# Kernel optimization log

Hardware: AMD Instinct MI355X
Metric: run time of the kernel (lower is better)

## Reference

```python
import jax, jax.numpy as jnp
import numpy as np


def _tet_geometry(vertices, indices, tet_density):
    """Gather 4 corners per tet, compute area (|det|/6), min edge length, alpha."""
    v = vertices[indices]                      # [T,4,3]
    v0, v1, v2, v3 = v[:, 0], v[:, 1], v[:, 2], v[:, 3]
    # --- tet area: |det([v1-v0, v2-v0, v3-v0])| / 6 ---
    e1, e2, e3 = v1 - v0, v2 - v0, v3 - v0     # [T,3] each
    det = (e1[:, 0] * (e2[:, 1] * e3[:, 2] - e2[:, 2] * e3[:, 1])
           - e1[:, 1] * (e2[:, 0] * e3[:, 2] - e2[:, 2] * e3[:, 0])
           + e1[:, 2] * (e2[:, 0] * e3[:, 1] - e2[:, 1] * e3[:, 0]))
    tet_area = jnp.abs(det) / 6.0              # [T]
    # --- edge lengths of all 6 edges, take min (mode='min') ---
    edge_sq = jnp.stack([
        jnp.sum((v0 - v1) ** 2, axis=1),
        jnp.sum((v0 - v2) ** 2, axis=1),
        jnp.sum((v0 - v3) ** 2, axis=1),
        jnp.sum((v1 - v2) ** 2, axis=1),
        jnp.sum((v1 - v3) ** 2, axis=1),
        jnp.sum((v2 - v3) ** 2, axis=1),
    ], axis=0)                                 # [6,T]
    el = jnp.sqrt(jnp.min(edge_sq, axis=0))    # [T]
    tet_alpha = 1.0 - jnp.exp(-tet_density * el)
    return tet_area, tet_alpha


def _vert_density(tet_density, indices, num_verts):
    # torch scatter_reduce_ 'amax' with zero-initialized dest and include_self=True
    # == segment_max over all 4 corner slots, clamped below at 0.
    flat_idx = indices.reshape(-1)                         # [4T]
    src = jnp.repeat(tet_density, 4)                       # [4T], matches row-major flatten
    vmax = jax.ops.segment_max(src, flat_idx, num_segments=num_verts)
    return jnp.maximum(vmax, jnp.zeros((), vmax.dtype))    # untouched verts -> 0


def setup_inputs() -> dict:
    key = jax.random.key(0)
    k1, k2, k3 = jax.random.split(key, 3)
    V, T = 1_000_000, 4_000_000
    vertices = jax.random.normal(k1, (V, 3), dtype=jnp.float32)
    indices = jax.random.randint(k2, (T, 4), 0, V, dtype=jnp.int32)
    tet_density = jax.random.uniform(k3, (T,), dtype=jnp.float32)
    return {"vertices": vertices, "indices": indices, "tet_density": tet_density}


def reference(vertices, indices, tet_density):
    tet_area, tet_alpha = _tet_geometry(vertices, indices, tet_density)
    vert_density = _vert_density(tet_density, indices, vertices.shape[0])
    return tet_area, tet_alpha, vert_density
```

## Files before the change

kernel.cpp:

```cpp
#include <hip/hip_runtime.h>

typedef int nt_int4 __attribute__((ext_vector_type(4)));

#define NB     256
#define VSHIFT 12
#define BMASK  ((1 << VSHIFT) - 1)
#define BCAP   65536
#define RT     4
#define NR     4


__global__ __launch_bounds__(256) void setup_kernel(uint4* __restrict__ vd4, int n4,
                                                    unsigned* __restrict__ gcnt,
                                                    const float* __restrict__ verts,
                                                    float4* __restrict__ verts4, int V) {
    int i = blockIdx.x * blockDim.x + threadIdx.x;
    if (i < n4) vd4[i] = make_uint4(0u, 0u, 0u, 0u);
    if (gcnt && i < NB) gcnt[i] = 0u;
    if (verts4 && i < V) {
        const float* p = verts + (size_t)i * 3;
        verts4[i] = make_float4(p[0], p[1], p[2], 0.f);
    }
}

__global__ __launch_bounds__(256) void fused_geom_bin_kernel(
    const float4* __restrict__ verts4,
    const int4*  __restrict__ idx4,
    const float* __restrict__ dens,
    float* __restrict__ out_area,
    float* __restrict__ out_alpha,
    unsigned*    __restrict__ pairs,
    unsigned*    __restrict__ gcnt,
    unsigned*    __restrict__ vd,
    int T)
{
    __shared__ unsigned s_cnt[NB];
    __shared__ unsigned s_run[NB];
    __shared__ unsigned s_roff[NB];
    __shared__ unsigned s_wc[NB];
    __shared__ unsigned s_wsum[4];
    __shared__ uint2    stage[256 * RT * 4];

    int tid  = threadIdx.x;
    int lane = tid & 63;
    int wid  = tid >> 6;
    int base = blockIdx.x * (256 * RT * NR);

    s_cnt[tid] = 0u;
    __syncthreads();
    for (int k = 0; k < RT * NR; ++k) {
        int i = base + k * 256 + tid;
        if (i < T) {
            int4 q = idx4[i];
            atomicAdd(&s_cnt[(unsigned)q.x >> VSHIFT], 1u);
            atomicAdd(&s_cnt[(unsigned)q.y >> VSHIFT], 1u);
            atomicAdd(&s_cnt[(unsigned)q.z >> VSHIFT], 1u);
            atomicAdd(&s_cnt[(unsigned)q.w >> VSHIFT], 1u);
        }
    }
    __syncthreads();

    s_run[tid] = atomicAdd(&gcnt[tid], s_cnt[tid]);
    __syncthreads();

    for (int r = 0; r < NR; ++r) {
        int4  q[RT];
        float dd[RT];
        bool  vl[RT];
#pragma unroll
        for (int k = 0; k < RT; ++k) {
            int i = base + (r * RT + k) * 256 + tid;
            vl[k] = (i < T);
            if (vl[k]) { q[k] = idx4[i]; dd[k] = dens[i]; }
        }

#pragma unroll
        for (int k = 0; k < RT; ++k) if (vl[k]) {
            int i = base + (r * RT + k) * 256 + tid;
            float4 v0 = verts4[q[k].x];
            float4 v1 = verts4[q[k].y];
            float4 v2 = verts4[q[k].z];
            float4 v3 = verts4[q[k].w];

            float e1x = v1.x - v0.x, e1y = v1.y - v0.y, e1z = v1.z - v0.z;
            float e2x = v2.x - v0.x, e2y = v2.y - v0.y, e2z = v2.z - v0.z;
            float e3x = v3.x - v0.x, e3y = v3.y - v0.y, e3z = v3.z - v0.z;

            float det = e1x * (e2y * e3z - e2z * e3y)
                      - e1y * (e2x * e3z - e2z * e3x)
                      + e1z * (e2x * e3y - e2y * e3x);
            __builtin_nontemporal_store(fabsf(det) * (1.0f / 6.0f), &out_area[i]);

            float q01 = e1x * e1x + e1y * e1y + e1z * e1z;
            float q02 = e2x * e2x + e2y * e2y + e2z * e2z;
            float q03 = e3x * e3x + e3y * e3y + e3z * e3z;
            float ax, ay, az;
            ax = v1.x - v2.x; ay = v1.y - v2.y; az = v1.z - v2.z;
            float q12 = ax * ax + ay * ay + az * az;
            ax = v1.x - v3.x; ay = v1.y - v3.y; az = v1.z - v3.z;
            float q13 = ax * ax + ay * ay + az * az;
            ax = v2.x - v3.x; ay = v2.y - v3.y; az = v2.z - v3.z;
            float q23 = ax * ax + ay * ay + az * az;

            float mn = fminf(fminf(fminf(q01, q02), fminf(q03, q12)), fminf(q13, q23));
            float el = sqrtf(mn);
            __builtin_nontemporal_store(1.0f - expf(-dd[k] * el), &out_alpha[i]);
        }

        s_cnt[tid] = 0u;
        __syncthreads();
#pragma unroll
        for (int k = 0; k < RT; ++k) if (vl[k]) {
            atomicAdd(&s_cnt[(unsigned)q[k].x >> VSHIFT], 1u);
            atomicAdd(&s_cnt[(unsigned)q[k].y >> VSHIFT], 1u);
            atomicAdd(&s_cnt[(unsigned)q[k].z >> VSHIFT], 1u);
            atomicAdd(&s_cnt[(unsigned)q[k].w >> VSHIFT], 1u);
        }
        __syncthreads();

        unsigned x = s_cnt[tid];
        unsigned incl = x;
#pragma unroll
        for (int s = 1; s < 64; s <<= 1) {
            unsigned t = __shfl_up(incl, s);
            if (lane >= s) incl += t;
        }
        if (lane == 63) s_wsum[wid] = incl;
        __syncthreads();
        unsigned pre = 0;
#pragma unroll
        for (int w = 0; w < 4; ++w) pre += (w < wid) ? s_wsum[w] : 0u;
        unsigned npairs = s_wsum[0] + s_wsum[1] + s_wsum[2] + s_wsum[3];
        s_roff[tid] = pre + incl - x;
        s_wc[tid]   = 0u;
        __syncthreads();

#pragma unroll
        for (int k = 0; k < RT; ++k) if (vl[k]) {
            unsigned db = __float_as_uint(dd[k]);
            unsigned vv[4] = { (unsigned)q[k].x, (unsigned)q[k].y,
                               (unsigned)q[k].z, (unsigned)q[k].w };
#pragma unroll
            for (int j = 0; j < 4; ++j) {
                unsigned b    = vv[j] >> VSHIFT;
                unsigned slot = s_roff[b] + atomicAdd(&s_wc[b], 1u);
                stage[slot] = make_uint2(vv[j], db);
            }
        }
        __syncthreads();

        for (unsigned l = tid; l < npairs; l += 256) {
            uint2 e = stage[l];
            unsigned b  = e.x >> VSHIFT;
            unsigned rr = s_run[b] + (l - s_roff[b]);
            if (rr < BCAP) {
                unsigned w = ((e.x & BMASK) << 20) | (e.y >> 12);
                __builtin_nontemporal_store(w, pairs + (size_t)b * BCAP + rr);
            } else {
                atomicMax(vd + e.x, e.y);
            }
        }
        __syncthreads();

        s_run[tid] += s_cnt[tid];
    }
}

__global__ __launch_bounds__(1024) void bucket_max_kernel(
    const unsigned* __restrict__ pairs,
    const unsigned* __restrict__ gcnt,
    unsigned*       __restrict__ vd,
    int V)
{
    __shared__ unsigned tbl[1 << VSHIFT];
    int b   = blockIdx.x;
    int tid = threadIdx.x;

    for (int j = tid; j < (1 << VSHIFT); j += 1024) tbl[j] = 0u;
    __syncthreads();

    unsigned cnt = gcnt[b];
    if (cnt > BCAP) cnt = BCAP;
    const unsigned* p = pairs + (size_t)b * BCAP;
    const uint4* p4 = (const uint4*)p;
    unsigned n4c = cnt >> 2;
    for (unsigned i = tid; i < n4c; i += 1024) {
        uint4 e = p4[i];
        atomicMax(&tbl[e.x >> 20], e.x << 12);
        atomicMax(&tbl[e.y >> 20], e.y << 12);
        atomicMax(&tbl[e.z >> 20], e.z << 12);
        atomicMax(&tbl[e.w >> 20], e.w << 12);
    }
    if (tid < (cnt & 3u)) {
        unsigned w = p[(cnt & ~3u) + tid];
        atomicMax(&tbl[w >> 20], w << 12);
    }
    __syncthreads();

    int vbase = b << VSHIFT;
    for (int j = tid; j < (1 << VSHIFT); j += 1024) {
        int v = vbase + j;
        if (v < V) {
            unsigned cur = vd[v];
            unsigned t   = tbl[j];
            vd[v] = cur > t ? cur : t;
        }
    }
}

__global__ __launch_bounds__(256) void tet_kernel_filter(
    const float4* __restrict__ verts4,
    const int*   __restrict__ indices,
    const float* __restrict__ density,
    float* __restrict__ out_area,
    float* __restrict__ out_alpha,
    unsigned int* __restrict__ vd,
    int T)
{
    int i = blockIdx.x * blockDim.x + threadIdx.x;
    if (i >= T) return;

    nt_int4 idx = __builtin_nontemporal_load((const nt_int4*)indices + i);
    float d     = __builtin_nontemporal_load(&density[i]);
    unsigned int db = __float_as_uint(d);

    unsigned int c0 = vd[idx.x];
    unsigned int c1 = vd[idx.y];
    unsigned int c2 = vd[idx.z];
    unsigned int c3 = vd[idx.w];

    float4 v0 = verts4[idx.x];
    float4 v1 = verts4[idx.y];
    float4 v2 = verts4[idx.z];
    float4 v3 = verts4[idx.w];

    float e1x = v1.x - v0.x, e1y = v1.y - v0.y, e1z = v1.z - v0.z;
    float e2x = v2.x - v0.x, e2y = v2.y - v0.y, e2z = v2.z - v0.z;
    float e3x = v3.x - v0.x, e3y = v3.y - v0.y, e3z = v3.z - v0.z;

    float det = e1x * (e2y * e3z - e2z * e3y)
              - e1y * (e2x * e3z - e2z * e3x)
              + e1z * (e2x * e3y - e2y * e3x);
    __builtin_nontemporal_store(fabsf(det) * (1.0f / 6.0f), &out_area[i]);

    float q01 = e1x * e1x + e1y * e1y + e1z * e1z;
    float q02 = e2x * e2x + e2y * e2y + e2z * e2z;
    float q03 = e3x * e3x + e3y * e3y + e3z * e3z;
    float ax, ay, az;
    ax = v1.x - v2.x; ay = v1.y - v2.y; az = v1.z - v2.z;
    float q12 = ax * ax + ay * ay + az * az;
    ax = v1.x - v3.x; ay = v1.y - v3.y; az = v1.z - v3.z;
    float q13 = ax * ax + ay * ay + az * az;
    ax = v2.x - v3.x; ay = v2.y - v3.y; az = v2.z - v3.z;
    float q23 = ax * ax + ay * ay + az * az;

    float mn = fminf(fminf(fminf(q01, q02), fminf(q03, q12)), fminf(q13, q23));
    float el = sqrtf(mn);
    __builtin_nontemporal_store(1.0f - expf(-d * el), &out_alpha[i]);

    if (db > c0) atomicMax(vd + idx.x, db);
    if (db > c1) atomicMax(vd + idx.y, db);
    if (db > c2) atomicMax(vd + idx.z, db);
    if (db > c3) atomicMax(vd + idx.w, db);
}

__global__ __launch_bounds__(256) void tet_kernel_fb(
    const float* __restrict__ verts,
    const int4*  __restrict__ indices,
    const float* __restrict__ density,
    float* __restrict__ out_area,
    float* __restrict__ out_alpha,
    unsigned int* __restrict__ vd,
    int T)
{
    int i = blockIdx.x * blockDim.x + threadIdx.x;
    if (i >= T) return;

    int4 idx = indices[i];
    float d = density[i];

    const float* p;
    p = verts + idx.x * 3; float v0x = p[0], v0y = p[1], v0z = p[2];
    p = verts + idx.y * 3; float v1x = p[0], v1y = p[1], v1z = p[2];
    p = verts + idx.z * 3; float v2x = p[0], v2y = p[1], v2z = p[2];
    p = verts + idx.w * 3; float v3x = p[0], v3y = p[1], v3z = p[2];

    float e1x = v1x - v0x, e1y = v1y - v0y, e1z = v1z - v0z;
    float e2x = v2x - v0x, e2y = v2y - v0y, e2z = v2z - v0z;
    float e3x = v3x - v0x, e3y = v3y - v0y, e3z = v3z - v0z;

    float det = e1x * (e2y * e3z - e2z * e3y)
              - e1y * (e2x * e3z - e2z * e3x)
              + e1z * (e2x * e3y - e2y * e3x);
    out_area[i] = fabsf(det) * (1.0f / 6.0f);

    float q01 = e1x * e1x + e1y * e1y + e1z * e1z;
    float q02 = e2x * e2x + e2y * e2y + e2z * e2z;
    float q03 = e3x * e3x + e3y * e3y + e3z * e3z;
    float ax, ay, az;
    ax = v1x - v2x; ay = v1y - v2y; az = v1z - v2z;
    float q12 = ax * ax + ay * ay + az * az;
    ax = v1x - v3x; ay = v1y - v3y; az = v1z - v3z;
    float q13 = ax * ax + ay * ay + az * az;
    ax = v2x - v3x; ay = v2y - v3y; az = v2z - v3z;
    float q23 = ax * ax + ay * ay + az * az;

    float mn = fminf(fminf(fminf(q01, q02), fminf(q03, q12)), fminf(q13, q23));
    float el = sqrtf(mn);
    out_alpha[i] = 1.0f - expf(-d * el);

    unsigned int db = __float_as_uint(d);
    atomicMax(vd + idx.x, db);
    atomicMax(vd + idx.y, db);
    atomicMax(vd + idx.z, db);
    atomicMax(vd + idx.w, db);
}


extern "C" void kernel_launch(void* const* d_in, const int* in_sizes, int n_in,
                              void* d_out, int out_size, void* d_ws, size_t ws_size,
                              hipStream_t stream) {
    const float* verts   = (const float*)d_in[0];
    const int*   indices = (const int*)d_in[1];
    const float* density = (const float*)d_in[2];
    int T = in_sizes[2];
    int V = in_sizes[0] / 3;

    float* out       = (float*)d_out;
    float* out_area  = out;
    float* out_alpha = out + (size_t)T;
    unsigned int* vd = (unsigned int*)(out + 2 * (size_t)T);

    const int block = 256;
    int n4 = V / 4;

    size_t pairsB = (size_t)NB * BCAP * sizeof(unsigned);
    size_t cntB   = (size_t)NB * sizeof(unsigned);
    size_t v4B    = (size_t)V * sizeof(float4);

    double mean = 4.0 * (double)T / NB;
    bool capOK = (mean + 12.0 * __builtin_sqrt(mean) <= (double)BCAP);
    bool fastOK = (V % 4 == 0) && (V <= (NB << VSHIFT)) && capOK && d_ws;

    int tetsPerBlock = block * RT * NR;
    int nbAct = (V + (1 << VSHIFT) - 1) >> VSHIFT;

    if (fastOK && ws_size >= pairsB + cntB + v4B) {
        unsigned* pairs  = (unsigned*)d_ws;
        unsigned* gcnt   = (unsigned*)((char*)d_ws + pairsB);
        float4*   verts4 = (float4*)((char*)d_ws + pairsB + ((cntB + 255) & ~(size_t)255));

        int setupN = (V > n4 ? V : n4);
        setup_kernel<<<(setupN + block - 1) / block, block, 0, stream>>>(
            (uint4*)vd, n4, gcnt, verts, verts4, V);

        fused_geom_bin_kernel<<<(T + tetsPerBlock - 1) / tetsPerBlock, block, 0, stream>>>(
            verts4, (const int4*)indices, density, out_area, out_alpha, pairs, gcnt, vd, T);

        bucket_max_kernel<<<nbAct, 1024, 0, stream>>>(pairs, gcnt, vd, V);
    } else if (d_ws && ws_size >= v4B && (V % 4) == 0) {
        float4* verts4 = (float4*)d_ws;
        int setupN = (V > n4 ? V : n4);
        setup_kernel<<<(setupN + block - 1) / block, block, 0, stream>>>(
            (uint4*)vd, n4, nullptr, verts, verts4, V);
        tet_kernel_filter<<<(T + block - 1) / block, block, 0, stream>>>(
            verts4, indices, density, out_area, out_alpha, vd, T);
    } else {
        setup_kernel<<<(n4 + block - 1) / block, block, 0, stream>>>(
            (uint4*)vd, n4, nullptr, nullptr, nullptr, 0);
        tet_kernel_fb<<<(T + block - 1) / block, block, 0, stream>>>(
            verts, (const int4*)indices, density, out_area, out_alpha, vd, T);
    }
}
```

Measured before the change: 412.9 us.

## Reserve global bucket slots per round and pad bucket counters

```diff
diff --git a/kernel.cpp b/kernel.cpp
--- a/kernel.cpp
+++ b/kernel.cpp
@@ -8,6 +8,7 @@
 #define BCAP   65536
 #define RT     4
 #define NR     4
+#define GPAD   16
 
 
 __global__ __launch_bounds__(256) void setup_kernel(uint4* __restrict__ vd4, int n4,
@@ -16,7 +17,7 @@
                                                     float4* __restrict__ verts4, int V) {
     int i = blockIdx.x * blockDim.x + threadIdx.x;
     if (i < n4) vd4[i] = make_uint4(0u, 0u, 0u, 0u);
-    if (gcnt && i < NB) gcnt[i] = 0u;
+    if (gcnt && i < NB * GPAD) gcnt[i] = 0u;
     if (verts4 && i < V) {
         const float* p = verts + (size_t)i * 3;
         verts4[i] = make_float4(p[0], p[1], p[2], 0.f);
@@ -35,7 +36,7 @@
     int T)
 {
     __shared__ unsigned s_cnt[NB];
-    __shared__ unsigned s_run[NB];
+    __shared__ unsigned s_base[NB];
     __shared__ unsigned s_roff[NB];
     __shared__ unsigned s_wc[NB];
     __shared__ unsigned s_wsum[4];
@@ -45,23 +46,6 @@
     int lane = tid & 63;
     int wid  = tid >> 6;
     int base = blockIdx.x * (256 * RT * NR);
-
-    s_cnt[tid] = 0u;
-    __syncthreads();
-    for (int k = 0; k < RT * NR; ++k) {
-        int i = base + k * 256 + tid;
-        if (i < T) {
-            int4 q = idx4[i];
-            atomicAdd(&s_cnt[(unsigned)q.x >> VSHIFT], 1u);
-            atomicAdd(&s_cnt[(unsigned)q.y >> VSHIFT], 1u);
-            atomicAdd(&s_cnt[(unsigned)q.z >> VSHIFT], 1u);
-            atomicAdd(&s_cnt[(unsigned)q.w >> VSHIFT], 1u);
-        }
-    }
-    __syncthreads();
-
-    s_run[tid] = atomicAdd(&gcnt[tid], s_cnt[tid]);
-    __syncthreads();
 
     for (int r = 0; r < NR; ++r) {
         int4  q[RT];
@@ -133,6 +117,7 @@
         unsigned npairs = s_wsum[0] + s_wsum[1] + s_wsum[2] + s_wsum[3];
         s_roff[tid] = pre + incl - x;
         s_wc[tid]   = 0u;
+        s_base[tid] = atomicAdd(&gcnt[tid * GPAD], x);
         __syncthreads();
 
 #pragma unroll
@@ -152,7 +137,7 @@
         for (unsigned l = tid; l < npairs; l += 256) {
             uint2 e = stage[l];
             unsigned b  = e.x >> VSHIFT;
-            unsigned rr = s_run[b] + (l - s_roff[b]);
+            unsigned rr = s_base[b] + (l - s_roff[b]);
             if (rr < BCAP) {
                 unsigned w = ((e.x & BMASK) << 20) | (e.y >> 12);
                 __builtin_nontemporal_store(w, pairs + (size_t)b * BCAP + rr);
@@ -161,8 +146,6 @@
             }
         }
         __syncthreads();
-
-        s_run[tid] += s_cnt[tid];
     }
 }
 
@@ -179,7 +162,7 @@
     for (int j = tid; j < (1 << VSHIFT); j += 1024) tbl[j] = 0u;
     __syncthreads();
 
-    unsigned cnt = gcnt[b];
+    unsigned cnt = gcnt[b * GPAD];
     if (cnt > BCAP) cnt = BCAP;
     const unsigned* p = pairs + (size_t)b * BCAP;
     const uint4* p4 = (const uint4*)p;
@@ -335,7 +318,7 @@
     int n4 = V / 4;
 
     size_t pairsB = (size_t)NB * BCAP * sizeof(unsigned);
-    size_t cntB   = (size_t)NB * sizeof(unsigned);
+    size_t cntB   = (size_t)NB * GPAD * sizeof(unsigned);
     size_t v4B    = (size_t)V * sizeof(float4);
 
     double mean = 4.0 * (double)T / NB;
@@ -345,7 +328,7 @@
     int tetsPerBlock = block * RT * NR;
     int nbAct = (V + (1 << VSHIFT) - 1) >> VSHIFT;
 
-    if (fastOK && ws_size >= pairsB + cntB + v4B) {
+    if (fastOK && ws_size >= pairsB + ((cntB + 255) & ~(size_t)255) + v4B) {
         unsigned* pairs  = (unsigned*)d_ws;
         unsigned* gcnt   = (unsigned*)((char*)d_ws + pairsB);
         float4*   verts4 = (float4*)((char*)d_ws + pairsB + ((cntB + 255) & ~(size_t)255));
```

Result: faster. 401.9 us (-2.7%).
